# Kernel tuning notes

Measured on AMD Instinct MI355X. Metric: run time of the kernel, lower is better.

The kernel has to match this reference:

```python
import jax, jax.numpy as jnp
import numpy as np

B, S, D, H = 4, 2048, 1024, 16
HD = D // H


def setup_inputs() -> dict:
    key = jax.random.key(0)
    k1, k2, k3 = jax.random.split(key, 3)
    x = jax.random.normal(k1, (B, S, D), dtype=jnp.float32)
    # xavier-ish scaling for stable softmax
    W_attn = jax.random.normal(k2, (3 * D, D), dtype=jnp.float32) * (1.0 / np.sqrt(2 * D))
    b_attn = jnp.zeros((3 * D,), dtype=jnp.float32)
    W_out = jax.random.normal(k3, (D, D), dtype=jnp.float32) * (1.0 / np.sqrt(D))
    b_out = jnp.zeros((D,), dtype=jnp.float32)
    return {"x": x, "W_attn": W_attn, "b_attn": b_attn, "W_out": W_out, "b_out": b_out}


def reference(x, W_attn, b_attn, W_out, b_out):
    bs, seq, d = x.shape
    # fused QKV projection (torch Linear: y = x @ W.T + b)
    kqv = jnp.einsum("bsd,ed->bse", x, W_attn) + b_attn
    # NOTE: source splits as k, q, v (k first)
    k, q, v = jnp.split(kqv, 3, axis=2)
    # [b, s, h, hd] -> [b, h, s, hd]
    k = k.reshape(bs, seq, H, HD).transpose(0, 2, 1, 3)
    q = q.reshape(bs, seq, H, HD).transpose(0, 2, 1, 3)
    v = v.reshape(bs, seq, H, HD).transpose(0, 2, 1, 3)
    scale = 1.0 / np.sqrt(HD)
    scores = jnp.einsum("bhqd,bhkd->bhqk", q, k) * scale
    attn = jax.nn.softmax(scores, axis=-1)
    y = jnp.einsum("bhqk,bhkd->bhqd", attn, v)
    y = y.transpose(0, 2, 1, 3).reshape(bs, seq, d)
    out = jnp.einsum("bsd,ed->bse", y, W_out) + b_out
    return out
```

## Files before the change

kernel.cpp:

```cpp
#include <hip/hip_runtime.h>

typedef unsigned short u16;
typedef unsigned int u32;
typedef __attribute__((ext_vector_type(2))) u32 u32x2;
typedef __attribute__((ext_vector_type(4))) u32 u32x4;
typedef __attribute__((ext_vector_type(8))) short bf16x8;
typedef __attribute__((ext_vector_type(4))) float f32x4;

__device__ __forceinline__ u16 f2bf(float f) {
  u32 b = __float_as_uint(f);
  b += 0x7fffu + ((b >> 16) & 1u);
  return (u16)(b >> 16);
}

__device__ __forceinline__ u32 pk2bf(float a, float b) {
#if __has_builtin(__builtin_amdgcn_cvt_pk_bf16_f32)
  return __builtin_bit_cast(u32, __builtin_amdgcn_cvt_pk_bf16_f32(a, b));
#else
  return (u32)f2bf(a) | ((u32)f2bf(b) << 16);
#endif
}

__device__ __forceinline__ float fexp2(float x) {
#if __has_builtin(__builtin_amdgcn_exp2f)
  return __builtin_amdgcn_exp2f(x);
#else
  return exp2f(x);
#endif
}

__device__ __forceinline__ void gload_lds16(const u16* g, u16* l) {
  __builtin_amdgcn_global_load_lds((const __attribute__((address_space(1))) void*)g,
                                   (__attribute__((address_space(3))) void*)l, 16, 0, 0);
}

__global__ __launch_bounds__(256) void cvt_f32_bf16(const float* __restrict__ in,
                                                    u16* __restrict__ out) {
  long i = ((long)blockIdx.x * 256 + threadIdx.x) * 8;
  u32 u[8];
#pragma unroll
  for (int j = 0; j < 8; j++) {
    u32 b = __float_as_uint(in[i + j]);
    u[j] = (b + 0x7fffu + ((b >> 16) & 1u)) >> 16;
  }
  u32x4 o;
  o[0] = u[0] | (u[1] << 16);
  o[1] = u[2] | (u[3] << 16);
  o[2] = u[4] | (u[5] << 16);
  o[3] = u[6] | (u[7] << 16);
  *(u32x4*)(out + i) = o;
}

__device__ __forceinline__ void gemm_core_128(const u16* __restrict__ A,
                                              const u16* __restrict__ B, int K,
                                              int m0, int n0, u16* As, u16* Bs,
                                              f32x4 acc[4][4]) {
  int t = threadIdx.x;
  int lane = t & 63, w = t >> 6;
  int quad = lane >> 4, l16 = lane & 15;
  int wm = (w >> 1) * 64, wn = (w & 1) * 64;
  int lr = lane >> 3, lc = lane & 7;
  int cg = lc ^ lr;
  int swz = l16 & 7;
  for (int k0 = 0; k0 < K; k0 += 64) {
#pragma unroll
    for (int i = 0; i < 4; i++) {
      int r0 = i * 32 + w * 8;
      gload_lds16(&A[(long)(m0 + r0 + lr) * K + k0 + cg * 8], &As[r0 * 64]);
      gload_lds16(&B[(long)(n0 + r0 + lr) * K + k0 + cg * 8], &Bs[r0 * 64]);
    }
    __syncthreads();
#pragma unroll
    for (int ks = 0; ks < 2; ks++) {
      bf16x8 a[4], b[4];
#pragma unroll
      for (int tm = 0; tm < 4; tm++)
        a[tm] = *(const bf16x8*)&As[(wm + tm * 16 + l16) * 64 + ((ks * 4 + quad) ^ swz) * 8];
#pragma unroll
      for (int tn = 0; tn < 4; tn++)
        b[tn] = *(const bf16x8*)&Bs[(wn + tn * 16 + l16) * 64 + ((ks * 4 + quad) ^ swz) * 8];
#pragma unroll
      for (int tm = 0; tm < 4; tm++)
#pragma unroll
        for (int tn = 0; tn < 4; tn++)
          acc[tm][tn] = __builtin_amdgcn_mfma_f32_16x16x32_bf16(a[tm], b[tn],
                                                                acc[tm][tn], 0, 0, 0);
    }
    __syncthreads();
  }
}

#define QSCALE 0.1803368801f
__global__ __launch_bounds__(256) void gemm_qkv(const u16* __restrict__ A,
                                                const u16* __restrict__ B,
                                                const float* __restrict__ bias,
                                                u16* __restrict__ Kg,
                                                u16* __restrict__ Qg,
                                                u16* __restrict__ Vg) {
  __shared__ __align__(16) u16 As[128 * 64];
  __shared__ __align__(16) u16 Bs[128 * 64];
  const int K = 1024;
  int m0 = blockIdx.y * 128, n0 = blockIdx.x * 128;
  f32x4 acc[4][4];
#pragma unroll
  for (int i = 0; i < 4; i++)
#pragma unroll
    for (int j = 0; j < 4; j++) acc[i][j] = (f32x4)0.0f;
  gemm_core_128(A, B, K, m0, n0, As, Bs, acc);

  int t = threadIdx.x, lane = t & 63, w = t >> 6;
  int quad = lane >> 4, l16 = lane & 15;
  int wm = (w >> 1) * 64, wn = (w & 1) * 64;
#pragma unroll
  for (int tn = 0; tn < 4; tn++) {
    int n = n0 + wn + tn * 16 + l16;
    float bv = bias[n];
    int which = n >> 10;
    int h = (n >> 6) & 15, d = n & 63;
#pragma unroll
    for (int tm = 0; tm < 4; tm++) {
      int m = m0 + wm + tm * 16 + quad * 4;
      int b = m >> 11, s = m & 2047;
      long bh = (long)b * 16 + h;
      if (which == 2) {
        u32x2 pk;
        pk[0] = pk2bf(acc[tm][tn][0] + bv, acc[tm][tn][1] + bv);
        pk[1] = pk2bf(acc[tm][tn][2] + bv, acc[tm][tn][3] + bv);
        *(u32x2*)&Vg[(bh * 64 + d) * 2048 + s] = pk;
      } else {
#pragma unroll
        for (int r = 0; r < 4; r++) {
          float v = acc[tm][tn][r] + bv;
          if (which == 0)
            Kg[(bh * 2048 + s + r) * 64 + d] = f2bf(v);
          else
            Qg[(bh * 2048 + s + r) * 64 + d] = f2bf(v * QSCALE);
        }
      }
    }
  }
}

__global__ __launch_bounds__(256) void gemm_out(const u16* __restrict__ A,
                                                const u16* __restrict__ B,
                                                const float* __restrict__ bias,
                                                float* __restrict__ out) {
  __shared__ __align__(16) u16 As[128 * 64];
  __shared__ __align__(16) u16 Bs[128 * 64];
  const int K = 1024, N = 1024;
  int m0 = blockIdx.y * 128, n0 = blockIdx.x * 128;
  f32x4 acc[4][4];
#pragma unroll
  for (int i = 0; i < 4; i++)
#pragma unroll
    for (int j = 0; j < 4; j++) acc[i][j] = (f32x4)0.0f;
  gemm_core_128(A, B, K, m0, n0, As, Bs, acc);

  int t = threadIdx.x, lane = t & 63, w = t >> 6;
  int quad = lane >> 4, l16 = lane & 15;
  int wm = (w >> 1) * 64, wn = (w & 1) * 64;
#pragma unroll
  for (int tn = 0; tn < 4; tn++) {
    int n = n0 + wn + tn * 16 + l16;
    float bv = bias[n];
#pragma unroll
    for (int tm = 0; tm < 4; tm++) {
#pragma unroll
      for (int r = 0; r < 4; r++) {
        int m = m0 + wm + tm * 16 + quad * 4 + r;
        out[(long)m * N + n] = acc[tm][tn][r] + bv;
      }
    }
  }
}

__global__ __launch_bounds__(256, 2) void attn_kernel(const u16* __restrict__ Qg,
                                                      const u16* __restrict__ Kg,
                                                      const u16* __restrict__ Vg,
                                                      u16* __restrict__ Y) {
  __shared__ __align__(16) u16 Ks[64 * 64];
  __shared__ __align__(16) u16 Vs[64 * 64];
  __shared__ __align__(16) u16 Ps[4 * 64 * 64];
  int t = threadIdx.x, lane = t & 63, w = t >> 6;
  int quad = lane >> 4, l16 = lane & 15;
  int bh = blockIdx.y;
  int q0 = blockIdx.x * 256 + w * 64;
  u16* Pw = Ps + w * 64 * 64;
  int lr = lane >> 3, lc = lane & 7, cg = lc ^ lr;
  int swz = l16 & 7;

  bf16x8 qf[4][2];
#pragma unroll
  for (int tq = 0; tq < 4; tq++) {
    const u16* qp = Qg + ((long)bh * 2048 + q0 + tq * 16 + l16) * 64;
    qf[tq][0] = *(const bf16x8*)(qp + quad * 8);
    qf[tq][1] = *(const bf16x8*)(qp + 32 + quad * 8);
  }

  float lsum[4] = {0.0f, 0.0f, 0.0f, 0.0f};
  f32x4 acc[4][4];
#pragma unroll
  for (int tn = 0; tn < 4; tn++)
#pragma unroll
    for (int tq = 0; tq < 4; tq++) acc[tn][tq] = (f32x4)0.0f;

  for (int kv0 = 0; kv0 < 2048; kv0 += 64) {
#pragma unroll
    for (int j = 0; j < 2; j++) {
      int r0 = j * 32 + w * 8;
      gload_lds16(&Kg[((long)bh * 2048 + kv0 + r0 + lr) * 64 + cg * 8], &Ks[r0 * 64]);
      gload_lds16(&Vg[((long)bh * 64 + r0 + lr) * 2048 + kv0 + cg * 8], &Vs[r0 * 64]);
    }
    __syncthreads();

    bf16x8 kf[4][2];
#pragma unroll
    for (int tn = 0; tn < 4; tn++)
#pragma unroll
      for (int ks = 0; ks < 2; ks++)
        kf[tn][ks] = *(const bf16x8*)&Ks[(tn * 16 + l16) * 64 + ((ks * 4 + quad) ^ swz) * 8];

#pragma unroll
    for (int tq = 0; tq < 4; tq++) {
      f32x4 s[4];
#pragma unroll
      for (int tn = 0; tn < 4; tn++) s[tn] = (f32x4)0.0f;
#pragma unroll
      for (int ks = 0; ks < 2; ks++)
#pragma unroll
        for (int tn = 0; tn < 4; tn++)
          s[tn] = __builtin_amdgcn_mfma_f32_16x16x32_bf16(kf[tn][ks], qf[tq][ks],
                                                          s[tn], 0, 0, 0);
      int qrow = tq * 16 + l16;
#pragma unroll
      for (int tn = 0; tn < 4; tn++) {
        float e0 = fexp2(s[tn][0]);
        float e1 = fexp2(s[tn][1]);
        float e2 = fexp2(s[tn][2]);
        float e3 = fexp2(s[tn][3]);
        lsum[tq] += (e0 + e1) + (e2 + e3);
        u32x2 pk;
        pk[0] = pk2bf(e0, e1);
        pk[1] = pk2bf(e2, e3);
        int c2 = ((tn * 2 + (quad >> 1)) ^ swz) * 2 + (quad & 1);
        *(u32x2*)&Pw[qrow * 64 + c2 * 4] = pk;
      }
    }

#pragma unroll
    for (int ks = 0; ks < 2; ks++) {
      bf16x8 vf[4];
#pragma unroll
      for (int tn = 0; tn < 4; tn++)
        vf[tn] = *(const bf16x8*)&Vs[(tn * 16 + l16) * 64 + ((ks * 4 + quad) ^ swz) * 8];
#pragma unroll
      for (int tq = 0; tq < 4; tq++) {
        bf16x8 pf = *(const bf16x8*)&Pw[(tq * 16 + l16) * 64 + ((ks * 4 + quad) ^ swz) * 8];
#pragma unroll
        for (int tn = 0; tn < 4; tn++)
          acc[tn][tq] = __builtin_amdgcn_mfma_f32_16x16x32_bf16(vf[tn], pf,
                                                                acc[tn][tq], 0, 0, 0);
      }
    }
    __syncthreads();
  }

#pragma unroll
  for (int tq = 0; tq < 4; tq++) {
    lsum[tq] += __shfl_xor(lsum[tq], 16, 64);
    lsum[tq] += __shfl_xor(lsum[tq], 32, 64);
  }

  int b = bh >> 4, h = bh & 15;
#pragma unroll
  for (int tq = 0; tq < 4; tq++) {
    float inv = 1.0f / lsum[tq];
    long row = (long)b * 2048 + q0 + tq * 16 + l16;
#pragma unroll
    for (int tn = 0; tn < 4; tn++) {
      u32x2 pk;
      pk[0] = pk2bf(acc[tn][tq][0] * inv, acc[tn][tq][1] * inv);
      pk[1] = pk2bf(acc[tn][tq][2] * inv, acc[tn][tq][3] * inv);
      *(u32x2*)&Y[row * 1024 + h * 64 + tn * 16 + quad * 4] = pk;
    }
  }
}

extern "C" void kernel_launch(void* const* d_in, const int* in_sizes, int n_in,
                              void* d_out, int out_size, void* d_ws, size_t ws_size,
                              hipStream_t stream) {
  const float* x = (const float*)d_in[0];
  const float* W_attn = (const float*)d_in[1];
  const float* b_attn = (const float*)d_in[2];
  const float* W_out = (const float*)d_in[3];
  const float* b_out = (const float*)d_in[4];
  float* out = (float*)d_out;

  char* ws = (char*)d_ws;
  u16* xb = (u16*)ws;
  u16* Wab = (u16*)(ws + 16777216);
  u16* Wob = (u16*)(ws + 16777216 + 6291456);
  u16* Kg = (u16*)(ws + 25165824);
  u16* Qg = Kg + 8388608;
  u16* Vg = Qg + 8388608;
  u16* Yb = xb;

  cvt_f32_bf16<<<4096, 256, 0, stream>>>(x, xb);
  cvt_f32_bf16<<<1536, 256, 0, stream>>>(W_attn, Wab);
  cvt_f32_bf16<<<512, 256, 0, stream>>>(W_out, Wob);

  gemm_qkv<<<dim3(24, 64), 256, 0, stream>>>(xb, Wab, b_attn, Kg, Qg, Vg);
  attn_kernel<<<dim3(8, 64), 256, 0, stream>>>(Qg, Kg, Vg, Yb);
  gemm_out<<<dim3(8, 64), 256, 0, stream>>>(Yb, Wob, b_out, out);
}
```

Before: 286.4 us.

## Swap GEMM operands, remap blocks per XCD, double-buffer attention KV tiles

Swaps the A/B operands in both GEMMs so each lane holds four consecutive output features, which lets the K/Q/out epilogues use vector stores and vector bias loads. V stores become scalar in exchange. Flattens the grids to 1D and remaps block indices so blocks landing on the same XCD share weight and activation tiles for L2 reuse. Double-buffers the K/V tiles in the attention kernel, prefetching the next tile while the current one is computed, so one barrier per iteration is removed. This doubles K/V LDS use, which may affect occupancy at two blocks per CU.

Measured after the change: 289.6 us. About the same (+1.1%).

```diff
diff --git a/kernel.cpp b/kernel.cpp
--- a/kernel.cpp
+++ b/kernel.cpp
@@ -91,8 +91,8 @@
 }
 
 #define QSCALE 0.1803368801f
-__global__ __launch_bounds__(256) void gemm_qkv(const u16* __restrict__ A,
-                                                const u16* __restrict__ B,
+__global__ __launch_bounds__(256) void gemm_qkv(const u16* __restrict__ W,
+                                                const u16* __restrict__ X,
                                                 const float* __restrict__ bias,
                                                 u16* __restrict__ Kg,
                                                 u16* __restrict__ Qg,
@@ -100,76 +100,87 @@
   __shared__ __align__(16) u16 As[128 * 64];
   __shared__ __align__(16) u16 Bs[128 * 64];
   const int K = 1024;
-  int m0 = blockIdx.y * 128, n0 = blockIdx.x * 128;
+  int lin = blockIdx.x;
+  int xcd = lin & 7, idx = lin >> 3;
+  int mb = (idx % 12) + 12 * (xcd & 1);
+  int sb = (idx / 12) + 16 * (xcd >> 1);
+  int m0 = mb * 128, n0 = sb * 128;
   f32x4 acc[4][4];
 #pragma unroll
   for (int i = 0; i < 4; i++)
 #pragma unroll
     for (int j = 0; j < 4; j++) acc[i][j] = (f32x4)0.0f;
-  gemm_core_128(A, B, K, m0, n0, As, Bs, acc);
+  gemm_core_128(W, X, K, m0, n0, As, Bs, acc);
 
   int t = threadIdx.x, lane = t & 63, w = t >> 6;
   int quad = lane >> 4, l16 = lane & 15;
   int wm = (w >> 1) * 64, wn = (w & 1) * 64;
-#pragma unroll
-  for (int tn = 0; tn < 4; tn++) {
-    int n = n0 + wn + tn * 16 + l16;
-    float bv = bias[n];
-    int which = n >> 10;
-    int h = (n >> 6) & 15, d = n & 63;
-#pragma unroll
-    for (int tm = 0; tm < 4; tm++) {
-      int m = m0 + wm + tm * 16 + quad * 4;
-      int b = m >> 11, s = m & 2047;
+  int which = m0 >> 10;
+#pragma unroll
+  for (int tm = 0; tm < 4; tm++) {
+    int nf0 = m0 + wm + tm * 16 + quad * 4;
+    int h = (nf0 >> 6) & 15, d0 = nf0 & 63;
+    f32x4 bv = *(const f32x4*)&bias[nf0];
+#pragma unroll
+    for (int tn = 0; tn < 4; tn++) {
+      int s_abs = n0 + wn + tn * 16 + l16;
+      int b = s_abs >> 11, s = s_abs & 2047;
       long bh = (long)b * 16 + h;
-      if (which == 2) {
+      f32x4 v;
+#pragma unroll
+      for (int r = 0; r < 4; r++) v[r] = acc[tm][tn][r] + bv[r];
+      if (which == 0) {
         u32x2 pk;
-        pk[0] = pk2bf(acc[tm][tn][0] + bv, acc[tm][tn][1] + bv);
-        pk[1] = pk2bf(acc[tm][tn][2] + bv, acc[tm][tn][3] + bv);
-        *(u32x2*)&Vg[(bh * 64 + d) * 2048 + s] = pk;
+        pk[0] = pk2bf(v[0], v[1]);
+        pk[1] = pk2bf(v[2], v[3]);
+        *(u32x2*)&Kg[(bh * 2048 + s) * 64 + d0] = pk;
+      } else if (which == 1) {
+        u32x2 pk;
+        pk[0] = pk2bf(v[0] * QSCALE, v[1] * QSCALE);
+        pk[1] = pk2bf(v[2] * QSCALE, v[3] * QSCALE);
+        *(u32x2*)&Qg[(bh * 2048 + s) * 64 + d0] = pk;
       } else {
 #pragma unroll
-        for (int r = 0; r < 4; r++) {
-          float v = acc[tm][tn][r] + bv;
-          if (which == 0)
-            Kg[(bh * 2048 + s + r) * 64 + d] = f2bf(v);
-          else
-            Qg[(bh * 2048 + s + r) * 64 + d] = f2bf(v * QSCALE);
-        }
+        for (int r = 0; r < 4; r++)
+          Vg[(bh * 64 + d0 + r) * 2048 + s] = f2bf(v[r]);
       }
     }
   }
 }
 
-__global__ __launch_bounds__(256) void gemm_out(const u16* __restrict__ A,
-                                                const u16* __restrict__ B,
+__global__ __launch_bounds__(256) void gemm_out(const u16* __restrict__ W,
+                                                const u16* __restrict__ Y,
                                                 const float* __restrict__ bias,
                                                 float* __restrict__ out) {
   __shared__ __align__(16) u16 As[128 * 64];
   __shared__ __align__(16) u16 Bs[128 * 64];
-  const int K = 1024, N = 1024;
-  int m0 = blockIdx.y * 128, n0 = blockIdx.x * 128;
+  const int K = 1024;
+  int lin = blockIdx.x;
+  int xcd = lin & 7, idx = lin >> 3;
+  int mb = idx & 7;
+  int sb = (idx >> 3) + 8 * xcd;
+  int m0 = mb * 128, n0 = sb * 128;
   f32x4 acc[4][4];
 #pragma unroll
   for (int i = 0; i < 4; i++)
 #pragma unroll
     for (int j = 0; j < 4; j++) acc[i][j] = (f32x4)0.0f;
-  gemm_core_128(A, B, K, m0, n0, As, Bs, acc);
+  gemm_core_128(W, Y, K, m0, n0, As, Bs, acc);
 
   int t = threadIdx.x, lane = t & 63, w = t >> 6;
   int quad = lane >> 4, l16 = lane & 15;
   int wm = (w >> 1) * 64, wn = (w & 1) * 64;
 #pragma unroll
-  for (int tn = 0; tn < 4; tn++) {
-    int n = n0 + wn + tn * 16 + l16;
-    float bv = bias[n];
-#pragma unroll
-    for (int tm = 0; tm < 4; tm++) {
-#pragma unroll
-      for (int r = 0; r < 4; r++) {
-        int m = m0 + wm + tm * 16 + quad * 4 + r;
-        out[(long)m * N + n] = acc[tm][tn][r] + bv;
-      }
+  for (int tm = 0; tm < 4; tm++) {
+    int nf0 = m0 + wm + tm * 16 + quad * 4;
+    f32x4 bv = *(const f32x4*)&bias[nf0];
+#pragma unroll
+    for (int tn = 0; tn < 4; tn++) {
+      int s_abs = n0 + wn + tn * 16 + l16;
+      f32x4 o;
+#pragma unroll
+      for (int r = 0; r < 4; r++) o[r] = acc[tm][tn][r] + bv[r];
+      *(f32x4*)&out[(long)s_abs * 1024 + nf0] = o;
     }
   }
 }
@@ -178,16 +189,21 @@
                                                       const u16* __restrict__ Kg,
                                                       const u16* __restrict__ Vg,
                                                       u16* __restrict__ Y) {
-  __shared__ __align__(16) u16 Ks[64 * 64];
-  __shared__ __align__(16) u16 Vs[64 * 64];
+  __shared__ __align__(16) u16 Ks[2][64 * 64];
+  __shared__ __align__(16) u16 Vs[2][64 * 64];
   __shared__ __align__(16) u16 Ps[4 * 64 * 64];
   int t = threadIdx.x, lane = t & 63, w = t >> 6;
   int quad = lane >> 4, l16 = lane & 15;
-  int bh = blockIdx.y;
-  int q0 = blockIdx.x * 256 + w * 64;
+  int lin = blockIdx.x;
+  int bh = (lin & 7) + (lin >> 6) * 8;
+  int qc = (lin >> 3) & 7;
+  int q0 = qc * 256 + w * 64;
   u16* Pw = Ps + w * 64 * 64;
   int lr = lane >> 3, lc = lane & 7, cg = lc ^ lr;
   int swz = l16 & 7;
+
+  const u16* Kbase = Kg + (long)bh * 2048 * 64;
+  const u16* Vbase = Vg + (long)bh * 64 * 2048;
 
   bf16x8 qf[4][2];
 #pragma unroll
@@ -204,21 +220,35 @@
 #pragma unroll
     for (int tq = 0; tq < 4; tq++) acc[tn][tq] = (f32x4)0.0f;
 
-  for (int kv0 = 0; kv0 < 2048; kv0 += 64) {
-#pragma unroll
-    for (int j = 0; j < 2; j++) {
-      int r0 = j * 32 + w * 8;
-      gload_lds16(&Kg[((long)bh * 2048 + kv0 + r0 + lr) * 64 + cg * 8], &Ks[r0 * 64]);
-      gload_lds16(&Vg[((long)bh * 64 + r0 + lr) * 2048 + kv0 + cg * 8], &Vs[r0 * 64]);
-    }
-    __syncthreads();
+#pragma unroll
+  for (int j = 0; j < 2; j++) {
+    int r0 = j * 32 + w * 8;
+    gload_lds16(&Kbase[(long)(r0 + lr) * 64 + cg * 8], &Ks[0][r0 * 64]);
+    gload_lds16(&Vbase[(long)(r0 + lr) * 2048 + cg * 8], &Vs[0][r0 * 64]);
+  }
+  __syncthreads();
+
+  for (int tile = 0; tile < 32; tile++) {
+    const u16* Kc = Ks[tile & 1];
+    const u16* Vc = Vs[tile & 1];
+    if (tile + 1 < 32) {
+      int kv0 = (tile + 1) * 64;
+      u16* Kn = Ks[(tile + 1) & 1];
+      u16* Vn = Vs[(tile + 1) & 1];
+#pragma unroll
+      for (int j = 0; j < 2; j++) {
+        int r0 = j * 32 + w * 8;
+        gload_lds16(&Kbase[(long)(kv0 + r0 + lr) * 64 + cg * 8], &Kn[r0 * 64]);
+        gload_lds16(&Vbase[(long)(r0 + lr) * 2048 + kv0 + cg * 8], &Vn[r0 * 64]);
+      }
+    }
 
     bf16x8 kf[4][2];
 #pragma unroll
     for (int tn = 0; tn < 4; tn++)
 #pragma unroll
       for (int ks = 0; ks < 2; ks++)
-        kf[tn][ks] = *(const bf16x8*)&Ks[(tn * 16 + l16) * 64 + ((ks * 4 + quad) ^ swz) * 8];
+        kf[tn][ks] = *(const bf16x8*)&Kc[(tn * 16 + l16) * 64 + ((ks * 4 + quad) ^ swz) * 8];
 
 #pragma unroll
     for (int tq = 0; tq < 4; tq++) {
@@ -252,7 +282,7 @@
       bf16x8 vf[4];
 #pragma unroll
       for (int tn = 0; tn < 4; tn++)
-        vf[tn] = *(const bf16x8*)&Vs[(tn * 16 + l16) * 64 + ((ks * 4 + quad) ^ swz) * 8];
+        vf[tn] = *(const bf16x8*)&Vc[(tn * 16 + l16) * 64 + ((ks * 4 + quad) ^ swz) * 8];
 #pragma unroll
       for (int tq = 0; tq < 4; tq++) {
         bf16x8 pf = *(const bf16x8*)&Pw[(tq * 16 + l16) * 64 + ((ks * 4 + quad) ^ swz) * 8];
@@ -309,7 +339,7 @@
   cvt_f32_bf16<<<1536, 256, 0, stream>>>(W_attn, Wab);
   cvt_f32_bf16<<<512, 256, 0, stream>>>(W_out, Wob);
 
-  gemm_qkv<<<dim3(24, 64), 256, 0, stream>>>(xb, Wab, b_attn, Kg, Qg, Vg);
-  attn_kernel<<<dim3(8, 64), 256, 0, stream>>>(Qg, Kg, Vg, Yb);
-  gemm_out<<<dim3(8, 64), 256, 0, stream>>>(Yb, Wob, b_out, out);
-}
+  gemm_qkv<<<1536, 256, 0, stream>>>(Wab, xb, b_attn, Kg, Qg, Vg);
+  attn_kernel<<<512, 256, 0, stream>>>(Qg, Kg, Vg, Yb);
+  gemm_out<<<512, 256, 0, stream>>>(Wob, Yb, b_out, out);
+}
```
